# Kernel tuning notes

Hardware: AMD Instinct MI355X
Metric: run time of the kernel (lower is better)

Reference implementation:

```python
import jax, jax.numpy as jnp
import numpy as np

N = 100_000      # nodes
E = 3_200_000    # edges (avg degree 32)
F_IN, H, C = 1433, 16, 7


def setup_inputs() -> dict:
    key = jax.random.key(0)
    ks = jax.random.split(key, 8)
    x = jax.random.normal(ks[0], (N, F_IN), jnp.float32)
    edge_index = jax.random.randint(ks[1], (2, E), 0, N, dtype=jnp.int32)
    s_in = 1.0 / np.sqrt(F_IN)
    s_h = 1.0 / np.sqrt(H)
    w_root1 = jax.random.normal(ks[2], (F_IN, H), jnp.float32) * s_in
    w_rel1 = jax.random.normal(ks[3], (F_IN, H), jnp.float32) * s_in
    b_rel1 = jnp.zeros((H,), jnp.float32)
    w_root2 = jax.random.normal(ks[4], (H, C), jnp.float32) * s_h
    w_rel2 = jax.random.normal(ks[5], (H, C), jnp.float32) * s_h
    b_rel2 = jnp.zeros((C,), jnp.float32)
    return {"x": x, "edge_index": edge_index,
            "w_root1": w_root1, "w_rel1": w_rel1, "b_rel1": b_rel1,
            "w_root2": w_root2, "w_rel2": w_rel2, "b_rel2": b_rel2}


def _graph_conv(x, src, dst, w_root, w_rel, b_rel, n_nodes):
    # GraphConv: out_i = W_root x_i + W_rel * sum_{j->i} x_j + b.
    # Sum-aggregation commutes with the linear map, so project first
    # (avoids gathering full-width features per edge).
    h = x @ w_rel                                   # [N, out]
    agg = jax.ops.segment_sum(h[src], dst, num_segments=n_nodes)  # [N, out]
    return agg + b_rel + x @ w_root


def reference(x, edge_index, w_root1, w_rel1, b_rel1, w_root2, w_rel2, b_rel2):
    src, dst = edge_index[0], edge_index[1]
    h1 = jax.nn.elu(_graph_conv(x, src, dst, w_root1, w_rel1, b_rel1, N))
    # F.dropout(training=self.training) -> identity in eval mode
    h2 = _graph_conv(h1, src, dst, w_root2, w_rel2, b_rel2, N)
    return jax.nn.log_softmax(h2, axis=1)
```

## Files before the change

kernel.cpp:

```cpp
#include <hip/hip_runtime.h>
#include <math.h>

#define FIN  1433
#define HID  16
#define NCLS 7
#define BM   128
#define BK   32
#define KS   4
#define KT_TOTAL 45

__global__ __launch_bounds__(256) void k1_gemm(
    const float* __restrict__ x,
    const float* __restrict__ w_root, const float* __restrict__ w_rel,
    const float* __restrict__ b_rel,
    float* __restrict__ pbase, float* __restrict__ abase,
    size_t seg_elems, int n) {
  __shared__ float xs[BK * BM];
  __shared__ float ws[BK * 32];

  const int tid   = threadIdx.x;
  const int row0  = blockIdx.x * BM;
  const int slice = blockIdx.y;
  const int cg    = tid & 7;
  const int rg    = tid >> 3;
  const int c0    = cg * 4;
  const int r0    = rg * 4;

  const int kt_beg = (KT_TOTAL * slice) / KS;
  const int kt_end = (KT_TOTAL * (slice + 1)) / KS;

  float acc[4][4];
#pragma unroll
  for (int i = 0; i < 4; ++i)
#pragma unroll
    for (int j = 0; j < 4; ++j) acc[i][j] = 0.f;

  float xreg[16], wreg[4];
  auto prefetch = [&](int kt) {
    const int k0 = kt * BK;
#pragma unroll
    for (int i = 0; i < 16; ++i) {
      int idx = i * 256 + tid;
      int r = idx >> 5, c = idx & 31;
      int gr = row0 + r, gk = k0 + c;
      xreg[i] = (gr < n && gk < FIN) ? x[(size_t)gr * FIN + gk] : 0.f;
    }
#pragma unroll
    for (int i = 0; i < 4; ++i) {
      int idx = i * 256 + tid;
      int kk = idx >> 5, c = idx & 31;
      int gk = k0 + kk;
      float v = 0.f;
      if (gk < FIN) v = (c < HID) ? w_rel[gk * HID + c] : w_root[gk * HID + (c - HID)];
      wreg[i] = v;
    }
  };

  prefetch(kt_beg);
  for (int kt = kt_beg; kt < kt_end; ++kt) {
    __syncthreads();
#pragma unroll
    for (int i = 0; i < 16; ++i) {
      int idx = i * 256 + tid;
      int r = idx >> 5, c = idx & 31;
      xs[c * BM + (r ^ c)] = xreg[i];
    }
#pragma unroll
    for (int i = 0; i < 4; ++i) {
      int idx = i * 256 + tid;
      int kk = idx >> 5, c = idx & 31;
      ws[kk * 32 + c] = wreg[i];
    }
    __syncthreads();
    if (kt + 1 < kt_end) prefetch(kt + 1);
#pragma unroll
    for (int kk = 0; kk < BK; ++kk) {
      float4 xv = *(const float4*)&xs[kk * BM + ((r0 ^ kk) & ~3)];
      float4 wv = *(const float4*)&ws[kk * 32 + c0];
      float comp[4] = {xv.x, xv.y, xv.z, xv.w};
      const int p = kk & 3;
      float xa[4] = {comp[0 ^ p], comp[1 ^ p], comp[2 ^ p], comp[3 ^ p]};
      float wa[4] = {wv.x, wv.y, wv.z, wv.w};
#pragma unroll
      for (int i = 0; i < 4; ++i)
#pragma unroll
        for (int j = 0; j < 4; ++j)
          acc[i][j] = fmaf(xa[i], wa[j], acc[i][j]);
    }
  }

  float* __restrict__ p_out = pbase + (size_t)slice * seg_elems;
  float* __restrict__ a_out = abase + (size_t)slice * seg_elems;
  if (cg < 4) {
#pragma unroll
    for (int i = 0; i < 4; ++i) {
      int gr = row0 + r0 + i;
      if (gr < n) {
        float4 v = {acc[i][0], acc[i][1], acc[i][2], acc[i][3]};
        *(float4*)&p_out[(size_t)gr * HID + c0] = v;
      }
    }
  } else {
    const int cb = c0 - HID;
    float b0 = 0.f, b1 = 0.f, b2v = 0.f, b3 = 0.f;
    if (slice == 0) { b0 = b_rel[cb]; b1 = b_rel[cb+1]; b2v = b_rel[cb+2]; b3 = b_rel[cb+3]; }
#pragma unroll
    for (int i = 0; i < 4; ++i) {
      int gr = row0 + r0 + i;
      if (gr < n) {
        float4 v = {acc[i][0] + b0, acc[i][1] + b1, acc[i][2] + b2v, acc[i][3] + b3};
        *(float4*)&a_out[(size_t)gr * HID + cb] = v;
      }
    }
  }
}

__global__ __launch_bounds__(256) void k_reduce(
    float* __restrict__ pbase, float* __restrict__ abase,
    size_t seg_elems, int n4) {
  int i = blockIdx.x * 256 + threadIdx.x;
  if (i >= n4) return;
  size_t s4 = seg_elems / 4;
  float4 a = ((const float4*)pbase)[i];
  float4 c = ((const float4*)abase)[i];
#pragma unroll
  for (int s = 1; s < KS; ++s) {
    float4 b = ((const float4*)pbase)[i + s * s4];
    float4 d = ((const float4*)abase)[i + s * s4];
    a.x += b.x; a.y += b.y; a.z += b.z; a.w += b.w;
    c.x += d.x; c.y += d.y; c.z += d.z; c.w += d.w;
  }
  ((float4*)pbase)[i] = a;
  ((float4*)abase)[i] = c;
}

__global__ __launch_bounds__(256) void k2_scatter16(
    const int* __restrict__ ei, const float* __restrict__ p,
    float* __restrict__ agg, int nE) {
  long long tid = (long long)blockIdx.x * 256 + threadIdx.x;
  if (tid >= (long long)nE * HID) return;
  int e = (int)(tid >> 4), f = (int)(tid & 15);
  int s = ei[e], d = ei[nE + e];
  unsafeAtomicAdd(agg + (size_t)d * HID + f, p[(size_t)s * HID + f]);
}

__global__ __launch_bounds__(256) void k3_l2(
    const float* __restrict__ agg,
    const float* __restrict__ w_root2, const float* __restrict__ w_rel2,
    const float* __restrict__ b2,
    float* __restrict__ p2, float* __restrict__ out2, int n) {
  int i = blockIdx.x * 256 + threadIdx.x;
  if (i >= n) return;
  const float4* a4 = (const float4*)(agg + (size_t)i * HID);
  float h[HID];
#pragma unroll
  for (int q = 0; q < 4; ++q) {
    float4 v = a4[q];
    float t[4] = {v.x, v.y, v.z, v.w};
#pragma unroll
    for (int j = 0; j < 4; ++j)
      h[4*q + j] = t[j] > 0.f ? t[j] : expm1f(t[j]);
  }
#pragma unroll
  for (int c = 0; c < NCLS; ++c) {
    float sr = 0.f, so = b2[c];
#pragma unroll
    for (int k = 0; k < HID; ++k) {
      sr = fmaf(h[k], w_rel2[k * NCLS + c], sr);
      so = fmaf(h[k], w_root2[k * NCLS + c], so);
    }
    p2[(size_t)i * NCLS + c] = sr;
    out2[(size_t)i * NCLS + c] = so;
  }
}

__global__ __launch_bounds__(256) void k4_scatter7(
    const int* __restrict__ ei, const float* __restrict__ p,
    float* __restrict__ out2, int nE) {
  long long tid = (long long)blockIdx.x * 256 + threadIdx.x;
  int e = (int)(tid >> 3), f = (int)(tid & 7);
  if (e >= nE || f >= NCLS) return;
  int s = ei[e], d = ei[nE + e];
  unsafeAtomicAdd(out2 + (size_t)d * NCLS + f, p[(size_t)s * NCLS + f]);
}

__global__ __launch_bounds__(256) void k5_lsm(float* __restrict__ out, int n) {
  int i = blockIdx.x * 256 + threadIdx.x;
  if (i >= n) return;
  float v[NCLS];
  float* o = out + (size_t)i * NCLS;
#pragma unroll
  for (int c = 0; c < NCLS; ++c) v[c] = o[c];
  float m = v[0];
#pragma unroll
  for (int c = 1; c < NCLS; ++c) m = fmaxf(m, v[c]);
  float s = 0.f;
#pragma unroll
  for (int c = 0; c < NCLS; ++c) s += expf(v[c] - m);
  float l = logf(s);
#pragma unroll
  for (int c = 0; c < NCLS; ++c) o[c] = v[c] - m - l;
}

extern "C" void kernel_launch(void* const* d_in, const int* in_sizes, int n_in,
                              void* d_out, int out_size, void* d_ws, size_t ws_size,
                              hipStream_t stream) {
  const float* x       = (const float*)d_in[0];
  const int*   ei      = (const int*)  d_in[1];
  const float* w_root1 = (const float*)d_in[2];
  const float* w_rel1  = (const float*)d_in[3];
  const float* b_rel1  = (const float*)d_in[4];
  const float* w_root2 = (const float*)d_in[5];
  const float* w_rel2  = (const float*)d_in[6];
  const float* b_rel2  = (const float*)d_in[7];
  float* out = (float*)d_out;

  int n  = in_sizes[0] / FIN;
  int nE = in_sizes[1] / 2;

  size_t seg = (size_t)n * HID;
  char* ws = (char*)d_ws;
  float* pbase = (float*)ws;
  float* abase = pbase + KS * seg;
  float* p2    = abase + KS * seg;

  int nbN = (n + 255) / 256;

  dim3 g1((n + BM - 1) / BM, KS);
  k1_gemm<<<g1, 256, 0, stream>>>(x, w_root1, w_rel1, b_rel1,
                                  pbase, abase, seg, n);
  int n4 = n * HID / 4;
  k_reduce<<<(n4 + 255) / 256, 256, 0, stream>>>(pbase, abase, seg, n4);

  long long t2 = (long long)nE * HID;
  k2_scatter16<<<(int)((t2 + 255) / 256), 256, 0, stream>>>(ei, pbase, abase, nE);

  k3_l2<<<nbN, 256, 0, stream>>>(abase, w_root2, w_rel2, b_rel2, p2, out, n);
  long long t4 = (long long)nE * 8;
  k4_scatter7<<<(int)((t4 + 255) / 256), 256, 0, stream>>>(ei, p2, out, nE);

  k5_lsm<<<nbN, 256, 0, stream>>>(out, n);
}
```

Baseline: 595.2 us.

## Use bf16 MFMA for first-layer projection GEMM with pre-transposed weights

```diff
diff --git a/kernel.cpp b/kernel.cpp
--- a/kernel.cpp
+++ b/kernel.cpp
@@ -1,4 +1,5 @@
 #include <hip/hip_runtime.h>
+#include <hip/hip_bf16.h>
 #include <math.h>
 
 #define FIN  1433
@@ -8,108 +9,106 @@
 #define BK   32
 #define KS   4
 #define KT_TOTAL 45
-
-__global__ __launch_bounds__(256) void k1_gemm(
-    const float* __restrict__ x,
+#define KPAD (KT_TOTAL * BK)
+
+typedef __attribute__((ext_vector_type(8))) short bf16x8;
+typedef __attribute__((ext_vector_type(4))) float f32x4;
+
+__global__ __launch_bounds__(256) void k_wt(
     const float* __restrict__ w_root, const float* __restrict__ w_rel,
+    ushort* __restrict__ wT) {
+  int idx = blockIdx.x * 256 + threadIdx.x;
+  if (idx >= 32 * KPAD) return;
+  int c = idx / KPAD, k = idx % KPAD;
+  float v = 0.f;
+  if (k < FIN) v = (c < HID) ? w_rel[k * HID + c] : w_root[k * HID + (c - HID)];
+  __hip_bfloat16 h = __float2bfloat16(v);
+  wT[idx] = *(ushort*)&h;
+}
+
+__global__ __launch_bounds__(256) void k1_mfma(
+    const float* __restrict__ x, const ushort* __restrict__ wT,
     const float* __restrict__ b_rel,
     float* __restrict__ pbase, float* __restrict__ abase,
-    size_t seg_elems, int n) {
-  __shared__ float xs[BK * BM];
-  __shared__ float ws[BK * 32];
-
-  const int tid   = threadIdx.x;
-  const int row0  = blockIdx.x * BM;
+    size_t seg, int n) {
+  __shared__ ushort xs[2][BM * BK];
+  __shared__ ushort wsh[2][32 * BK];
+
+  const int tid  = threadIdx.x;
+  const int lane = tid & 63;
+  const int wave = tid >> 6;
+  const int row0 = blockIdx.x * BM;
   const int slice = blockIdx.y;
-  const int cg    = tid & 7;
-  const int rg    = tid >> 3;
-  const int c0    = cg * 4;
-  const int r0    = rg * 4;
-
   const int kt_beg = (KT_TOTAL * slice) / KS;
   const int kt_end = (KT_TOTAL * (slice + 1)) / KS;
 
-  float acc[4][4];
-#pragma unroll
-  for (int i = 0; i < 4; ++i)
-#pragma unroll
-    for (int j = 0; j < 4; ++j) acc[i][j] = 0.f;
-
-  float xreg[16], wreg[4];
-  auto prefetch = [&](int kt) {
+  f32x4 acc[2][2] = {};
+
+  const int sr  = tid >> 5;
+  const int sk  = tid & 31;
+  const int wc  = tid >> 3;
+  const int wt4 = tid & 7;
+
+  float  xr[16];
+  ushort4 wr;
+
+  auto load_tile = [&](int kt) {
     const int k0 = kt * BK;
+    const int gk = k0 + sk;
+    const bool kv = gk < FIN;
 #pragma unroll
     for (int i = 0; i < 16; ++i) {
-      int idx = i * 256 + tid;
-      int r = idx >> 5, c = idx & 31;
-      int gr = row0 + r, gk = k0 + c;
-      xreg[i] = (gr < n && gk < FIN) ? x[(size_t)gr * FIN + gk] : 0.f;
-    }
-#pragma unroll
-    for (int i = 0; i < 4; ++i) {
-      int idx = i * 256 + tid;
-      int kk = idx >> 5, c = idx & 31;
-      int gk = k0 + kk;
-      float v = 0.f;
-      if (gk < FIN) v = (c < HID) ? w_rel[gk * HID + c] : w_root[gk * HID + (c - HID)];
-      wreg[i] = v;
-    }
+      int gr = row0 + i * 8 + sr;
+      xr[i] = (gr < n && kv) ? x[(size_t)gr * FIN + gk] : 0.f;
+    }
+    wr = *(const ushort4*)&wT[(size_t)wc * KPAD + k0 + wt4 * 4];
   };
 
-  prefetch(kt_beg);
-  for (int kt = kt_beg; kt < kt_end; ++kt) {
+  auto store_stage = [&](int b) {
+#pragma unroll
+    for (int i = 0; i < 16; ++i) {
+      __hip_bfloat16 h = __float2bfloat16(xr[i]);
+      xs[b][(i * 8 + sr) * BK + sk] = *(ushort*)&h;
+    }
+    *(ushort4*)&wsh[b][wc * BK + wt4 * 4] = wr;
+  };
+
+  const int m = lane & 15, o = lane >> 4;
+
+  auto do_mfma = [&](int b) {
+    bf16x8 b0 = *(const bf16x8*)&wsh[b][(m)      * BK + o * 8];
+    bf16x8 b1 = *(const bf16x8*)&wsh[b][(16 + m) * BK + o * 8];
+#pragma unroll
+    for (int mf = 0; mf < 2; ++mf) {
+      bf16x8 a = *(const bf16x8*)&xs[b][(wave * 32 + mf * 16 + m) * BK + o * 8];
+      acc[mf][0] = __builtin_amdgcn_mfma_f32_16x16x32_bf16(a, b0, acc[mf][0], 0, 0, 0);
+      acc[mf][1] = __builtin_amdgcn_mfma_f32_16x16x32_bf16(a, b1, acc[mf][1], 0, 0, 0);
+    }
+  };
+
+  load_tile(kt_beg);
+  store_stage(0);
+  __syncthreads();
+  for (int t = kt_beg; t < kt_end; ++t) {
+    const int b = (t - kt_beg) & 1;
+    const bool more = (t + 1) < kt_end;
+    if (more) load_tile(t + 1);
+    do_mfma(b);
+    if (more) store_stage(b ^ 1);
     __syncthreads();
-#pragma unroll
-    for (int i = 0; i < 16; ++i) {
-      int idx = i * 256 + tid;
-      int r = idx >> 5, c = idx & 31;
-      xs[c * BM + (r ^ c)] = xreg[i];
-    }
-#pragma unroll
-    for (int i = 0; i < 4; ++i) {
-      int idx = i * 256 + tid;
-      int kk = idx >> 5, c = idx & 31;
-      ws[kk * 32 + c] = wreg[i];
-    }
-    __syncthreads();
-    if (kt + 1 < kt_end) prefetch(kt + 1);
-#pragma unroll
-    for (int kk = 0; kk < BK; ++kk) {
-      float4 xv = *(const float4*)&xs[kk * BM + ((r0 ^ kk) & ~3)];
-      float4 wv = *(const float4*)&ws[kk * 32 + c0];
-      float comp[4] = {xv.x, xv.y, xv.z, xv.w};
-      const int p = kk & 3;
-      float xa[4] = {comp[0 ^ p], comp[1 ^ p], comp[2 ^ p], comp[3 ^ p]};
-      float wa[4] = {wv.x, wv.y, wv.z, wv.w};
-#pragma unroll
-      for (int i = 0; i < 4; ++i)
-#pragma unroll
-        for (int j = 0; j < 4; ++j)
-          acc[i][j] = fmaf(xa[i], wa[j], acc[i][j]);
-    }
-  }
-
-  float* __restrict__ p_out = pbase + (size_t)slice * seg_elems;
-  float* __restrict__ a_out = abase + (size_t)slice * seg_elems;
-  if (cg < 4) {
-#pragma unroll
-    for (int i = 0; i < 4; ++i) {
-      int gr = row0 + r0 + i;
+  }
+
+  float* __restrict__ p_out = pbase + (size_t)slice * seg;
+  float* __restrict__ a_out = abase + (size_t)slice * seg;
+  const float bv = (slice == 0) ? b_rel[m] : 0.f;
+#pragma unroll
+  for (int mf = 0; mf < 2; ++mf) {
+#pragma unroll
+    for (int j = 0; j < 4; ++j) {
+      int gr = row0 + wave * 32 + mf * 16 + o * 4 + j;
       if (gr < n) {
-        float4 v = {acc[i][0], acc[i][1], acc[i][2], acc[i][3]};
-        *(float4*)&p_out[(size_t)gr * HID + c0] = v;
-      }
-    }
-  } else {
-    const int cb = c0 - HID;
-    float b0 = 0.f, b1 = 0.f, b2v = 0.f, b3 = 0.f;
-    if (slice == 0) { b0 = b_rel[cb]; b1 = b_rel[cb+1]; b2v = b_rel[cb+2]; b3 = b_rel[cb+3]; }
-#pragma unroll
-    for (int i = 0; i < 4; ++i) {
-      int gr = row0 + r0 + i;
-      if (gr < n) {
-        float4 v = {acc[i][0] + b0, acc[i][1] + b1, acc[i][2] + b2v, acc[i][3] + b3};
-        *(float4*)&a_out[(size_t)gr * HID + cb] = v;
+        p_out[(size_t)gr * HID + m] = acc[mf][0][j];
+        a_out[(size_t)gr * HID + m] = acc[mf][1][j] + bv;
       }
     }
   }
@@ -220,15 +219,17 @@
 
   size_t seg = (size_t)n * HID;
   char* ws = (char*)d_ws;
-  float* pbase = (float*)ws;
-  float* abase = pbase + KS * seg;
-  float* p2    = abase + KS * seg;
+  float*  pbase = (float*)ws;
+  float*  abase = pbase + KS * seg;
+  float*  p2    = abase + KS * seg;
+  ushort* wT    = (ushort*)(p2 + (size_t)n * NCLS);
 
   int nbN = (n + 255) / 256;
 
+  k_wt<<<(32 * KPAD + 255) / 256, 256, 0, stream>>>(w_root1, w_rel1, wT);
+
   dim3 g1((n + BM - 1) / BM, KS);
-  k1_gemm<<<g1, 256, 0, stream>>>(x, w_root1, w_rel1, b_rel1,
-                                  pbase, abase, seg, n);
+  k1_mfma<<<g1, 256, 0, stream>>>(x, wT, b_rel1, pbase, abase, seg, n);
   int n4 = n * HID / 4;
   k_reduce<<<(n4 + 255) / 256, 256, 0, stream>>>(pbase, abase, seg, n4);
 
```

Measured after the change: 555.9 us. 6.6% less time.
